# Optimization experiments

Hardware: AMD Instinct MI355X
Metric: run time of the kernel (lower is better)

## Reference

```python
import jax, jax.numpy as jnp
import numpy as np

B, C, H, W = 4, 512, 64, 64
CI = C // 2  # inter_channel


def setup_inputs() -> dict:
    key = jax.random.key(0)
    ks = jax.random.split(key, 5)
    x = jax.random.normal(ks[0], (B, C, H, W), dtype=jnp.float32)
    # 1x1 convs with bias=False == channel-mixing matrices (out_ch, in_ch)
    w_phi = jax.random.normal(ks[1], (CI, C), dtype=jnp.float32) * 0.02
    w_theta = jax.random.normal(ks[2], (CI, C), dtype=jnp.float32) * 0.02
    w_g = jax.random.normal(ks[3], (CI, C), dtype=jnp.float32) * 0.02
    w_mask = jax.random.normal(ks[4], (C, CI), dtype=jnp.float32) * 0.02
    return {"x": x, "w_phi": w_phi, "w_theta": w_theta, "w_g": w_g, "w_mask": w_mask}


def reference(x, w_phi, w_theta, w_g, w_mask):
    b, c, h, w = x.shape
    n = h * w
    ci = w_phi.shape[0]
    xf = x.reshape(b, c, n)  # (b, c, N)
    # 1x1 convs as channel matmuls -> (b, ci, N)
    phi = jnp.einsum('oc,bcn->bon', w_phi, xf)
    theta = jnp.einsum('oc,bcn->bon', w_theta, xf)
    g = jnp.einsum('oc,bcn->bon', w_g, xf)
    # f = theta^T @ phi : (b, N, N), unscaled scores
    f = jnp.einsum('bcn,bcm->bnm', theta, phi)
    a = jax.nn.softmax(f, axis=-1)
    # y = a @ g^T, produced directly in (b, ci, N) layout (fuses the permute)
    y = jnp.einsum('bnm,bcm->bcn', a, g)
    # conv_mask: 1x1 conv back to C channels
    out = jnp.einsum('oc,bcn->bon', w_mask, y)
    return out.reshape(b, c, h, w)
```

## Files before the change

### kernel.cpp

```cpp
#include <hip/hip_runtime.h>


#define BB 4
#define CC 512
#define NN_SP 4096
#define CI 256

typedef _Float16 f16x8 __attribute__((ext_vector_type(8)));
typedef float f32x4 __attribute__((ext_vector_type(4)));

__device__ __forceinline__ void async16(const void* gsrc, void* ldst) {
  __builtin_amdgcn_global_load_lds(
      (const __attribute__((address_space(1))) unsigned int*)gsrc,
      (__attribute__((address_space(3))) unsigned int*)ldst, 16, 0, 0);
}

__global__ __launch_bounds__(256) void transpose_convert(
    const float* __restrict__ x, _Float16* __restrict__ xT,
    const float* __restrict__ wphi, const float* __restrict__ wtheta,
    const float* __restrict__ wg, const float* __restrict__ wmask,
    _Float16* __restrict__ wpt, _Float16* __restrict__ wgh, _Float16* __restrict__ wmh) {
  __shared__ float tile[64][65];
  const int n0 = blockIdx.x * 64, c0 = blockIdx.y * 64, b = blockIdx.z;
  const int tx = threadIdx.x & 63, ty = threadIdx.x >> 6;
  const float* xb = x + (long long)b * CC * NN_SP;
#pragma unroll
  for (int i = 0; i < 16; ++i) {
    int row = i * 4 + ty;
    tile[row][tx] = xb[(long long)(c0 + row) * NN_SP + n0 + tx];
  }
  __syncthreads();
  const int cx = threadIdx.x & 31;
  const int ny = threadIdx.x >> 5;
  _Float16* xTb = xT + (long long)b * NN_SP * CC;
#pragma unroll
  for (int i = 0; i < 8; ++i) {
    int n = i * 8 + ny;
    union { _Float16 h[2]; unsigned int u; } pk;
    pk.h[0] = (_Float16)tile[cx * 2][n];
    pk.h[1] = (_Float16)tile[cx * 2 + 1][n];
    *(unsigned int*)(xTb + (long long)(n0 + n) * CC + c0 + cx * 2) = pk.u;
  }
  const int blid = blockIdx.x + blockIdx.y * 64 + blockIdx.z * 512;
  const int i = blid * 256 + threadIdx.x;
  if (i < 512 * 512) {
    int row = i >> 9, k = i & 511;
    float v = (row < 256) ? wphi[row * 512 + k] : wtheta[(row - 256) * 512 + k];
    wpt[i] = (_Float16)v;
  } else if (i < 512 * 512 + 256 * 512) {
    int j = i - 512 * 512;
    wgh[j] = (_Float16)wg[j];
  } else {
    int j = i - 512 * 512 - 256 * 512;
    wmh[j] = (_Float16)wmask[j];
  }
}

template <int M, int NT, int K, bool F16OUT>
__global__ __launch_bounds__(256, 2) void gemm_bt(
    const _Float16* __restrict__ Ab, const _Float16* __restrict__ Btb,
    void* __restrict__ Cb, long long sA, long long sB, long long sC) {
  __shared__ _Float16 As[128 * 64];
  __shared__ _Float16 Bs[128 * 64];
  const int tid = threadIdx.x, lane = tid & 63, w = tid >> 6;
  const int wm = w >> 1, wn = w & 1;
  const int l15 = lane & 15, lq = lane >> 4;
  const int b = blockIdx.z;
  const _Float16* A = Ab + (long long)b * sA;
  const _Float16* Bt = Btb + (long long)b * sB;
  const int m0 = blockIdx.y * 128, n0 = blockIdx.x * 128;

  f32x4 acc[4][4];
#pragma unroll
  for (int i = 0; i < 4; ++i)
#pragma unroll
    for (int j = 0; j < 4; ++j) acc[i][j] = (f32x4){0.f, 0.f, 0.f, 0.f};

  for (int k0 = 0; k0 < K; k0 += 64) {
    __syncthreads();
#pragma unroll
    for (int j = 0; j < 4; ++j) {
      int chw = j * 256 + w * 64;
      int ch = chw + lane;
      int us = ch ^ ((ch >> 3) & 7);
      int row = us >> 3, kc = us & 7;
      async16(A + (long long)(m0 + row) * K + k0 + kc * 8, (void*)(As + chw * 8));
      async16(Bt + (long long)(n0 + row) * K + k0 + kc * 8, (void*)(Bs + chw * 8));
    }
    __syncthreads();
#pragma unroll
    for (int kh = 0; kh < 2; ++kh) {
      f16x8 af[4], bf[4];
#pragma unroll
      for (int mt = 0; mt < 4; ++mt) {
        int c = (wm * 64 + mt * 16 + l15) * 8 + kh * 4 + lq;
        af[mt] = *(const f16x8*)(As + (c ^ ((c >> 3) & 7)) * 8);
      }
#pragma unroll
      for (int nt = 0; nt < 4; ++nt) {
        int c = (wn * 64 + nt * 16 + l15) * 8 + kh * 4 + lq;
        bf[nt] = *(const f16x8*)(Bs + (c ^ ((c >> 3) & 7)) * 8);
      }
#pragma unroll
      for (int mt = 0; mt < 4; ++mt)
#pragma unroll
        for (int nt = 0; nt < 4; ++nt)
          acc[mt][nt] = __builtin_amdgcn_mfma_f32_16x16x32_f16(af[mt], bf[nt], acc[mt][nt], 0, 0, 0);
    }
  }

#pragma unroll
  for (int mt = 0; mt < 4; ++mt)
#pragma unroll
    for (int nt = 0; nt < 4; ++nt)
#pragma unroll
      for (int r = 0; r < 4; ++r) {
        int row = m0 + wm * 64 + mt * 16 + lq * 4 + r;
        int col = n0 + wn * 64 + nt * 16 + l15;
        if (F16OUT)
          ((_Float16*)Cb + (long long)b * sC)[(long long)row * NT + col] = (_Float16)acc[mt][nt][r];
        else
          ((float*)Cb + (long long)b * sC)[(long long)row * NT + col] = acc[mt][nt][r];
      }
}

__global__ __launch_bounds__(512, 2) void flash_attn3(
    const _Float16* __restrict__ pt, const _Float16* __restrict__ g,
    _Float16* __restrict__ yT) {
  __shared__ _Float16 Stg[2][2][16384];
  __shared__ _Float16 Ps[8][2048];
  const int tid = threadIdx.x, lane = tid & 63, w = tid >> 6;
  const int hw = w >> 2, wp = w & 3;
  const int l15 = lane & 15, lq = lane >> 4;

  const int idx = blockIdx.x;
  const int b = (idx >> 1) & 3;
  const int q0 = (((idx >> 3) << 1) | (idx & 1)) * 64;
  const int kvbase = hw * 2048;
  const _Float16* __restrict__ ptb = pt + (long long)b * NN_SP * 512;
  const _Float16* __restrict__ gb = g + (long long)b * CI * NN_SP;

  int offPhi[4], offG[4], chw_[4];
#pragma unroll
  for (int j = 0; j < 4; ++j) {
    int u = wp * 256 + j * 64 + lane;
    chw_[j] = wp * 256 + j * 64;
    int us = u ^ ((u >> 3) & 7);
    int k2 = us >> 9, nv8 = (us >> 6) & 7, r15 = (us >> 2) & 15, rq = us & 3;
    offPhi[j] = (nv8 * 16 + r15) * 512 + k2 * 32 + rq * 8;
    int kq = us >> 8, ct4 = (us >> 6) & 3;
    offG[j] = (ct4 * 16 + r15) * 4096 + kq * 32 + rq * 8;
  }
  const int rswz = (l15 * 4 + lq) ^ ((l15 >> 1) & 7);

  f16x8 qreg[8];
#pragma unroll
  for (int kk = 0; kk < 8; ++kk)
    qreg[kk] = *(const f16x8*)(
        ptb + (long long)(q0 + wp * 16 + l15) * 512 + 256 + kk * 32 + lq * 8);

  f16x8 onesf;
#pragma unroll
  for (int j = 0; j < 8; ++j) onesf[j] = (_Float16)1.f;

  f32x4 yacc[16];
#pragma unroll
  for (int nt = 0; nt < 16; ++nt) yacc[nt] = (f32x4){0.f, 0.f, 0.f, 0.f};
  f32x4 lacc = (f32x4){0.f, 0.f, 0.f, 0.f};
  float mrow[4] = {-3e38f, -3e38f, -3e38f, -3e38f};

  auto issue = [&](int mq, int bi) {
    if (mq >= 64) return;
    int t = mq >> 2, mp = mq & 3, kv0 = kvbase + t * 128;
#pragma unroll
    for (int hh = 0; hh < 2; ++hh) {
      int sub = mp * 2 + hh;
      _Float16* buf = Stg[hw][bi] + hh * 8192;
      if (sub < 4) {
        const _Float16* basep = ptb + (long long)kv0 * 512 + sub * 64;
#pragma unroll
        for (int j = 0; j < 4; ++j)
          async16(basep + offPhi[j], (void*)(buf + chw_[j] * 8));
      } else {
        const _Float16* baseg = gb + (long long)(sub - 4) * 64 * 4096 + kv0;
#pragma unroll
        for (int j = 0; j < 4; ++j)
          async16(baseg + offG[j], (void*)(buf + chw_[j] * 8));
      }
    }
  };

  int p = 0;
  issue(0, 0);

  for (int t = 0; t < 16; ++t) {
    f32x4 S[8];
#pragma unroll
    for (int i = 0; i < 8; ++i) S[i] = (f32x4){0.f, 0.f, 0.f, 0.f};

#pragma unroll
    for (int mp = 0; mp < 2; ++mp) {
      asm volatile("s_waitcnt vmcnt(0)" ::: "memory");
      asm volatile("s_barrier" ::: "memory");
      issue(p + 1, (p + 1) & 1);
      const _Float16* bufb = Stg[hw][p & 1];
      __builtin_amdgcn_s_setprio(1);
#pragma unroll
      for (int hh = 0; hh < 2; ++hh) {
        int c = mp * 2 + hh;
        const _Float16* buf = bufb + hh * 8192;
#pragma unroll
        for (int k2 = 0; k2 < 2; ++k2)
#pragma unroll
          for (int nv = 0; nv < 8; ++nv) {
            f16x8 bf = *(const f16x8*)(buf + (k2 * 512 + nv * 64 + rswz) * 8);
            S[nv] = __builtin_amdgcn_mfma_f32_16x16x32_f16(qreg[c * 2 + k2], bf, S[nv], 0, 0, 0);
          }
      }
      __builtin_amdgcn_s_setprio(0);
      ++p;
    }

    float nm[4];
    int grew = 0;
#pragma unroll
    for (int r = 0; r < 4; ++r) {
      float mx = fmaxf(fmaxf(S[0][r], S[1][r]), fmaxf(S[2][r], S[3][r]));
      mx = fmaxf(mx, fmaxf(fmaxf(S[4][r], S[5][r]), fmaxf(S[6][r], S[7][r])));
#pragma unroll
      for (int d = 1; d < 16; d <<= 1) mx = fmaxf(mx, __shfl_xor(mx, d, 64));
      nm[r] = fmaxf(mrow[r], mx);
      grew |= (mx > mrow[r]);
    }
    if (__ballot(grew)) {
      f32x4 al;
#pragma unroll
      for (int r = 0; r < 4; ++r) {
        al[r] = __expf(mrow[r] - nm[r]);
        mrow[r] = nm[r];
      }
#pragma unroll
      for (int nt = 0; nt < 16; ++nt) yacc[nt] *= al;
      lacc *= al;
    }
#pragma unroll
    for (int r = 0; r < 4; ++r)
#pragma unroll
      for (int nv = 0; nv < 8; ++nv) S[nv][r] = __expf(S[nv][r] - mrow[r]);

#pragma unroll
    for (int nv = 0; nv < 8; ++nv) {
      int kq = nv >> 1;
      int lqr = (nv & 1) * 2 + (l15 >> 3);
      int e = l15 & 7;
#pragma unroll
      for (int r = 0; r < 4; ++r) {
        int u = kq * 64 + lqr * 16 + lq * 4 + r;
        int us = u ^ ((u >> 3) & 7);
        Ps[w][us * 8 + e] = (_Float16)S[nv][r];
      }
    }
    f16x8 aP[4];
#pragma unroll
    for (int kq = 0; kq < 4; ++kq) {
      int ur = kq * 64 + lane;
      int urs = ur ^ ((ur >> 3) & 7);
      aP[kq] = *(const f16x8*)(&Ps[w][urs * 8]);
    }

#pragma unroll
    for (int kq = 0; kq < 4; ++kq)
      lacc = __builtin_amdgcn_mfma_f32_16x16x32_f16(aP[kq], onesf, lacc, 0, 0, 0);

#pragma unroll
    for (int mp = 0; mp < 2; ++mp) {
      asm volatile("s_waitcnt vmcnt(0)" ::: "memory");
      asm volatile("s_barrier" ::: "memory");
      issue(p + 1, (p + 1) & 1);
      const _Float16* bufb = Stg[hw][p & 1];
      __builtin_amdgcn_s_setprio(1);
#pragma unroll
      for (int hh = 0; hh < 2; ++hh) {
        int cg = mp * 2 + hh;
        const _Float16* buf = bufb + hh * 8192;
#pragma unroll
        for (int kq = 0; kq < 4; ++kq)
#pragma unroll
          for (int ct = 0; ct < 4; ++ct) {
            f16x8 bf = *(const f16x8*)(buf + (kq * 256 + ct * 64 + rswz) * 8);
            yacc[cg * 4 + ct] =
                __builtin_amdgcn_mfma_f32_16x16x32_f16(aP[kq], bf, yacc[cg * 4 + ct], 0, 0, 0);
          }
      }
      __builtin_amdgcn_s_setprio(0);
      ++p;
    }
  }

  __syncthreads();
  float* mbuf = (float*)Stg;
  float* sbuf = (float*)((char*)Stg + 81920);
  if (hw == 1) {
#pragma unroll
    for (int r = 0; r < 4; ++r) {
      int rr = wp * 16 + lq * 4 + r;
#pragma unroll
      for (int nt = 0; nt < 16; ++nt)
        mbuf[rr * 257 + nt * 16 + l15] = yacc[nt][r];
      if (l15 == 0) {
        sbuf[rr * 2 + 0] = mrow[r];
        sbuf[rr * 2 + 1] = lacc[r];
      }
    }
  }
  __syncthreads();
  if (hw == 0) {
    _Float16* yTb = yT + (long long)b * NN_SP * CI;
#pragma unroll
    for (int r = 0; r < 4; ++r) {
      int rr = wp * 16 + lq * 4 + r;
      float m2 = sbuf[rr * 2 + 0], l2 = sbuf[rr * 2 + 1];
      float m = fmaxf(mrow[r], m2);
      float w1 = __expf(mrow[r] - m), w2 = __expf(m2 - m);
      float inv = 1.f / (w1 * lacc[r] + w2 * l2);
      int row = q0 + rr;
#pragma unroll
      for (int nt = 0; nt < 16; ++nt) {
        float v2 = mbuf[rr * 257 + nt * 16 + l15];
        yTb[(long long)row * CI + nt * 16 + l15] =
            (_Float16)((w1 * yacc[nt][r] + w2 * v2) * inv);
      }
    }
  }
}

extern "C" void kernel_launch(void* const* d_in, const int* in_sizes, int n_in,
                              void* d_out, int out_size, void* d_ws, size_t ws_size,
                              hipStream_t stream) {
  const float* x = (const float*)d_in[0];
  const float* w_phi = (const float*)d_in[1];
  const float* w_theta = (const float*)d_in[2];
  const float* w_g = (const float*)d_in[3];
  const float* w_mask = (const float*)d_in[4];
  float* out = (float*)d_out;
  char* ws = (char*)d_ws;

  _Float16* xT = (_Float16*)(ws);
  _Float16* pt = (_Float16*)(ws + 16777216);
  _Float16* gB = (_Float16*)(ws + 33554432);
  _Float16* yT = (_Float16*)(ws + 41943040);
  _Float16* wpt = (_Float16*)(ws + 50331648);
  _Float16* wg = (_Float16*)(ws + 50855936);
  _Float16* wm = (_Float16*)(ws + 51118080);

  transpose_convert<<<dim3(64, 8, 4), 256, 0, stream>>>(
      x, xT, w_phi, w_theta, w_g, w_mask, wpt, wg, wm);
  gemm_bt<4096, 512, 512, true><<<dim3(4, 32, 4), 256, 0, stream>>>(
      xT, wpt, pt, 4096LL * 512, 0, 4096LL * 512);
  gemm_bt<256, 4096, 512, true><<<dim3(32, 2, 4), 256, 0, stream>>>(
      wg, xT, gB, 0, 4096LL * 512, 256LL * 4096);
  flash_attn3<<<dim3(256), 512, 0, stream>>>(pt, gB, yT);
  gemm_bt<512, 4096, 256, false><<<dim3(32, 4, 4), 256, 0, stream>>>(
      wm, yT, out, 0, 4096LL * 256, 512LL * 4096);
}
```

Baseline: 245.5 us.

## Fuse output 1x1 conv projection into flash attention epilogue

After the attention merge, the normalized Y tile (64 queries x 256 channels) is written into shared memory in a swizzled layout instead of going to global memory. All eight waves then run MFMA against the fp16 mask weights read directly from global memory and write fp32 output. This removes the yT round trip and one kernel launch. The cost is extra epilogue work per block, uncached global weight loads repeated across 256 blocks, and uncoalesced 16-float strided stores.

Measured after the change: 242.6 us. No clear change (-1.2%).

```diff
diff --git a/kernel.cpp b/kernel.cpp
--- a/kernel.cpp
+++ b/kernel.cpp
@@ -126,7 +126,7 @@
 
 __global__ __launch_bounds__(512, 2) void flash_attn3(
     const _Float16* __restrict__ pt, const _Float16* __restrict__ g,
-    _Float16* __restrict__ yT) {
+    const _Float16* __restrict__ wmh, float* __restrict__ out) {
   __shared__ _Float16 Stg[2][2][16384];
   __shared__ _Float16 Ps[8][2048];
   const int tid = threadIdx.x, lane = tid & 63, w = tid >> 6;
@@ -300,6 +300,7 @@
   __syncthreads();
   float* mbuf = (float*)Stg;
   float* sbuf = (float*)((char*)Stg + 81920);
+  _Float16* Yb = (_Float16*)Ps;
   if (hw == 1) {
 #pragma unroll
     for (int r = 0; r < 4; ++r) {
@@ -315,7 +316,6 @@
   }
   __syncthreads();
   if (hw == 0) {
-    _Float16* yTb = yT + (long long)b * NN_SP * CI;
 #pragma unroll
     for (int r = 0; r < 4; ++r) {
       int rr = wp * 16 + lq * 4 + r;
@@ -323,14 +323,50 @@
       float m = fmaxf(mrow[r], m2);
       float w1 = __expf(mrow[r] - m), w2 = __expf(m2 - m);
       float inv = 1.f / (w1 * lacc[r] + w2 * l2);
-      int row = q0 + rr;
 #pragma unroll
       for (int nt = 0; nt < 16; ++nt) {
         float v2 = mbuf[rr * 257 + nt * 16 + l15];
-        yTb[(long long)row * CI + nt * 16 + l15] =
-            (_Float16)((w1 * yacc[nt][r] + w2 * v2) * inv);
-      }
-    }
+        _Float16 yv = (_Float16)((w1 * yacc[nt][r] + w2 * v2) * inv);
+        int u = (lq * 4 + r) * 4 + (nt & 1) * 2 + (l15 >> 3);
+        int us = u ^ ((u >> 3) & 7);
+        Yb[(((nt >> 1) * 4 + wp) * 64 + us) * 8 + (l15 & 7)] = yv;
+      }
+    }
+  }
+  __syncthreads();
+
+  {
+    f32x4 oacc[4][4];
+#pragma unroll
+    for (int i = 0; i < 4; ++i)
+#pragma unroll
+      for (int j = 0; j < 4; ++j) oacc[i][j] = (f32x4){0.f, 0.f, 0.f, 0.f};
+#pragma unroll
+    for (int kk = 0; kk < 8; ++kk) {
+      f16x8 aw[4], by[4];
+#pragma unroll
+      for (int mt = 0; mt < 4; ++mt)
+        aw[mt] = *(const f16x8*)(wmh + (w * 64 + mt * 16 + l15) * 256 + kk * 32 + lq * 8);
+#pragma unroll
+      for (int nt = 0; nt < 4; ++nt)
+        by[nt] = *(const f16x8*)(Yb + ((kk * 4 + nt) * 64 + rswz) * 8);
+#pragma unroll
+      for (int mt = 0; mt < 4; ++mt)
+#pragma unroll
+        for (int nt = 0; nt < 4; ++nt)
+          oacc[mt][nt] = __builtin_amdgcn_mfma_f32_16x16x32_f16(aw[mt], by[nt], oacc[mt][nt], 0, 0, 0);
+    }
+    float* outb = out + (long long)b * CC * NN_SP;
+#pragma unroll
+    for (int mt = 0; mt < 4; ++mt)
+#pragma unroll
+      for (int nt = 0; nt < 4; ++nt)
+#pragma unroll
+        for (int r = 0; r < 4; ++r) {
+          int o = w * 64 + mt * 16 + lq * 4 + r;
+          int n = nt * 16 + l15;
+          outb[(long long)o * NN_SP + q0 + n] = oacc[mt][nt][r];
+        }
   }
 }
 
@@ -348,7 +384,6 @@
   _Float16* xT = (_Float16*)(ws);
   _Float16* pt = (_Float16*)(ws + 16777216);
   _Float16* gB = (_Float16*)(ws + 33554432);
-  _Float16* yT = (_Float16*)(ws + 41943040);
   _Float16* wpt = (_Float16*)(ws + 50331648);
   _Float16* wg = (_Float16*)(ws + 50855936);
   _Float16* wm = (_Float16*)(ws + 51118080);
@@ -359,7 +394,5 @@
       xT, wpt, pt, 4096LL * 512, 0, 4096LL * 512);
   gemm_bt<256, 4096, 512, true><<<dim3(32, 2, 4), 256, 0, stream>>>(
       wg, xT, gB, 0, 4096LL * 512, 256LL * 4096);
-  flash_attn3<<<dim3(256), 512, 0, stream>>>(pt, gB, yT);
-  gemm_bt<512, 4096, 256, false><<<dim3(32, 4, 4), 256, 0, stream>>>(
-      wm, yT, out, 0, 4096LL * 256, 512LL * 4096);
-}
+  flash_attn3<<<dim3(256), 512, 0, stream>>>(pt, gB, wm, out);
+}
```
